# Kernel optimization log

Measured on AMD Instinct MI355X. Metric: run time of the kernel, lower is better.

Reference implementation:

```python
import jax, jax.numpy as jnp
import numpy as np

EPS = 1e-5

def conv1x1(x, W, b):
    # x: [B,C,H,W], W: [O,C], b: [O] -- a 1x1 conv is a per-pixel matmul
    return jnp.einsum('bchw,oc->bohw', x, W) + b[None, :, None, None]

def mean_variance_norm(feat):
    # torch .var(dim=2) is unbiased (ddof=1)
    m = feat.mean(axis=(2, 3), keepdims=True)
    v = feat.var(axis=(2, 3), ddof=1, keepdims=True)
    return (feat - m) / jnp.sqrt(v + EPS)

def setup_inputs() -> dict:
    key = jax.random.key(0)
    ks = jax.random.split(key, 10)
    B, C, H, W = 4, 256, 64, 64
    sc = 1.0 / np.sqrt(C)
    return {
        'content': jax.random.normal(ks[0], (B, C, H, W), jnp.float32),
        'style': jax.random.normal(ks[1], (B, C, H, W), jnp.float32),
        'content_key': jax.random.normal(ks[2], (B, C, H, W), jnp.float32),
        'style_key': jax.random.normal(ks[3], (B, C, H, W), jnp.float32),
        'Wf': jax.random.normal(ks[4], (C, C), jnp.float32) * sc,
        'bf': jnp.zeros((C,), jnp.float32),
        'Wg': jax.random.normal(ks[5], (C, C), jnp.float32) * sc,
        'bg': jnp.zeros((C,), jnp.float32),
        'Wh': jax.random.normal(ks[6], (C, C), jnp.float32) * sc,
        'bh': jnp.zeros((C,), jnp.float32),
    }

def reference(content, style, content_key, style_key, Wf, bf, Wg, bg, Wh, bh):
    Fq = conv1x1(content_key, Wf, bf)   # [B,Ck,H,W]
    G = conv1x1(style_key, Wg, bg)      # [B,Ck,Hs,Ws]
    Hv = conv1x1(style, Wh, bh)         # [B,C,Hs,Ws]
    b, _, h, w = Fq.shape
    _, C, hs, ws = Hv.shape
    N, M = h * w, hs * ws
    q = Fq.reshape(b, -1, N).transpose(0, 2, 1)   # [B,N,Ck]
    k = G.reshape(b, -1, M)                        # [B,Ck,M]
    style_flat = Hv.reshape(b, C, M).transpose(0, 2, 1)  # [B,M,C]
    # masks are all-ones -> attn_mask all zeros -> no masking (faithful to None path)
    S = jax.nn.softmax(jnp.einsum('bnc,bcm->bnm', q, k), axis=-1)  # [B,N,M]
    mean = jnp.einsum('bnm,bmc->bnc', S, style_flat)               # [B,N,C]
    std = jnp.sqrt(jax.nn.relu(
        jnp.einsum('bnm,bmc->bnc', S, style_flat * style_flat) - mean * mean))
    mean = mean.reshape(b, h, w, C).transpose(0, 3, 1, 2)  # [B,C,H,W]
    std = std.reshape(b, h, w, C).transpose(0, 3, 1, 2)
    return std * mean_variance_norm(content) + mean
```

## Files before the change

kernel.cpp:

```cpp
#include <hip/hip_runtime.h>


typedef unsigned int u32;
typedef unsigned short u16;
typedef _Float16 f16x8 __attribute__((ext_vector_type(8)));
typedef float f32x4 __attribute__((ext_vector_type(4)));
typedef float f32x16 __attribute__((ext_vector_type(16)));

#define L2E 1.44269504088896340736f
#define MFMA(a, b, c) __builtin_amdgcn_mfma_f32_16x16x32_f16(a, b, c, 0, 0, 0)
#define MFMA32(a, b, c) __builtin_amdgcn_mfma_f32_32x32x16_f16(a, b, c, 0, 0, 0)
#define EXP2(x) __builtin_amdgcn_exp2f(x)

__device__ __forceinline__ u16 h_bits(_Float16 h) { return __builtin_bit_cast(u16, h); }
__device__ __forceinline__ _Float16 bits_h(u16 x) { return __builtin_bit_cast(_Float16, x); }
__device__ __forceinline__ u16 f2h(float f) { return h_bits((_Float16)f); }

__device__ __forceinline__ f16x8 ldh8(const u16* p) {
    uint4 v = *(const uint4*)p;
    return __builtin_bit_cast(f16x8, v);
}

__global__ void k_stats(const float* __restrict__ content,
                        float* __restrict__ cm, float* __restrict__ cr) {
    int blk = blockIdx.x;
    const float* p = content + (size_t)blk * 4096;
    int t = threadIdx.x;
    float s = 0.f, ss = 0.f;
    for (int i = 0; i < 4; i++) {
        float4 v = *(const float4*)(p + (i * 256 + t) * 4);
        s  += (v.x + v.y) + (v.z + v.w);
        ss += (v.x * v.x + v.y * v.y) + (v.z * v.z + v.w * v.w);
    }
    for (int d = 32; d >= 1; d >>= 1) { s += __shfl_xor(s, d); ss += __shfl_xor(ss, d); }
    __shared__ __align__(16) float as[4], ass[4];
    int w = t >> 6;
    if ((t & 63) == 0) { as[w] = s; ass[w] = ss; }
    __syncthreads();
    if (t == 0) {
        s  = (as[0] + as[1]) + (as[2] + as[3]);
        ss = (ass[0] + ass[1]) + (ass[2] + ass[3]);
        float mean = s * (1.0f / 4096.0f);
        float var = (ss - s * mean) * (1.0f / 4095.0f);
        cm[blk] = mean;
        cr[blk] = rsqrtf(var + 1e-5f);
    }
}

__global__ void k_prep(const float* __restrict__ style, const float* __restrict__ ckey,
                       const float* __restrict__ skey,
                       const float* __restrict__ Wf, const float* __restrict__ Wg,
                       const float* __restrict__ Wh,
                       u16* __restrict__ A, u16* __restrict__ Xq, u16* __restrict__ Cc,
                       u16* __restrict__ Wb) {
    int z = blockIdx.z, t = threadIdx.x;
    if (z >= 12) {
        if (blockIdx.y != 0) return;
        int m = z - 12;
        const float* src = (m == 0) ? Wf : ((m == 1) ? Wg : Wh);
        u16* dst = Wb + m * 65536;
        int i = (blockIdx.x * 256 + t) * 4;
        float4 v = *(const float4*)(src + i);
        ushort4 o;
        o.x = f2h(v.x); o.y = f2h(v.y); o.z = f2h(v.z); o.w = f2h(v.w);
        *(ushort4*)(dst + i) = o;
        return;
    }
    int tensor = z >> 2, b = z & 3;
    const float* src = ((tensor == 0) ? style : ((tensor == 1) ? ckey : skey))
                       + (size_t)b * 256 * 4096;
    u16* dst = ((tensor == 0) ? A : ((tensor == 1) ? Xq : Cc)) + (size_t)b * 4096 * 256;
    int c0 = blockIdx.y * 64, t0 = blockIdx.x * 64;
    __shared__ __align__(16) float ls[64][65];
    int tr = t >> 4, tc = t & 15;
    for (int i = 0; i < 4; i++) {
        int c_off = i * 16 + tr;
        float4 v = *(const float4*)(src + (size_t)(c0 + c_off) * 4096 + t0 + tc * 4);
        ls[tc * 4 + 0][c_off] = v.x;
        ls[tc * 4 + 1][c_off] = v.y;
        ls[tc * 4 + 2][c_off] = v.z;
        ls[tc * 4 + 3][c_off] = v.w;
    }
    __syncthreads();
    for (int i = 0; i < 4; i++) {
        int tokrow = i * 16 + tr;
        ushort4 o;
        o.x = f2h(ls[tokrow][tc * 4 + 0]);
        o.y = f2h(ls[tokrow][tc * 4 + 1]);
        o.z = f2h(ls[tokrow][tc * 4 + 2]);
        o.w = f2h(ls[tokrow][tc * 4 + 3]);
        *(ushort4*)(dst + (size_t)(t0 + tokrow) * 256 + c0 + tc * 4) = o;
    }
}

__launch_bounds__(256, 2)
__global__ void k_gemm_qk(const u16* Xqs, u16* Qd, u16* Xk, const u16* __restrict__ Wb,
                          const float* __restrict__ bfp, const float* __restrict__ bgp) {
    int mode = blockIdx.z, b = blockIdx.y, tok0 = blockIdx.x * 128;
    const u16* X = ((mode == 0) ? Xqs : Xk) + (size_t)b * 4096 * 256;
    u16* O = ((mode == 0) ? Qd : Xk) + (size_t)b * 4096 * 256;
    const u16* W = Wb + mode * 65536;
    const float* bias = (mode == 0) ? bfp : bgp;
    __shared__ __align__(16) u16 wt[256 * 40];
    int t = threadIdx.x, w = t >> 6, lane = t & 63, ln = lane & 15, quad = lane >> 4;

    f32x4 acc[8][4];
    for (int i = 0; i < 8; i++)
        for (int j = 0; j < 4; j++) acc[i][j] = f32x4{0.f, 0.f, 0.f, 0.f};

    for (int ks = 0; ks < 8; ks++) {
        {
            const u16* wr = W + t * 256 + ks * 32;
            uint4 w0 = *(const uint4*)(wr + 0);
            uint4 w1 = *(const uint4*)(wr + 8);
            uint4 w2 = *(const uint4*)(wr + 16);
            uint4 w3 = *(const uint4*)(wr + 24);
            *(uint4*)(wt + t * 40 + 0)  = w0;
            *(uint4*)(wt + t * 40 + 8)  = w1;
            *(uint4*)(wt + t * 40 + 16) = w2;
            *(uint4*)(wt + t * 40 + 24) = w3;
        }
        __syncthreads();
        f16x8 wf[4];
        #pragma unroll
        for (int ct = 0; ct < 4; ct++)
            wf[ct] = ldh8(wt + (w * 64 + ct * 16 + ln) * 40 + quad * 8);
        #pragma unroll
        for (int rt = 0; rt < 8; rt++) {
            f16x8 xf = ldh8(X + (size_t)(tok0 + rt * 16 + ln) * 256 + ks * 32 + quad * 8);
            #pragma unroll
            for (int ct = 0; ct < 4; ct++) acc[rt][ct] = MFMA(xf, wf[ct], acc[rt][ct]);
        }
        __syncthreads();
    }

    float bv[4];
    #pragma unroll
    for (int ct = 0; ct < 4; ct++) bv[ct] = bias[w * 64 + ct * 16 + ln];
    #pragma unroll
    for (int rt = 0; rt < 8; rt++)
        #pragma unroll
        for (int ct = 0; ct < 4; ct++)
            #pragma unroll
            for (int r = 0; r < 4; r++) {
                int tok = tok0 + rt * 16 + quad * 4 + r;
                int o = w * 64 + ct * 16 + ln;
                O[(size_t)tok * 256 + o] = f2h(acc[rt][ct][r] + bv[ct]);
            }
}

__launch_bounds__(256, 2)
__global__ void k_gemm_v(const u16* Xs, const u16* __restrict__ Wh2,
                         const float* __restrict__ bhp, u16* Vt) {
    int b = blockIdx.y, tok0 = blockIdx.x * 128;
    const u16* X = Xs + (size_t)b * 4096 * 256;
    __shared__ __align__(16) u16 wt[256 * 40];
    int t = threadIdx.x, w = t >> 6, lane = t & 63, ln = lane & 15, quad = lane >> 4;

    f32x4 acc[8][4];
    for (int i = 0; i < 8; i++)
        for (int j = 0; j < 4; j++) acc[i][j] = f32x4{0.f, 0.f, 0.f, 0.f};

    for (int ks = 0; ks < 8; ks++) {
        {
            const u16* wr = Wh2 + t * 256 + ks * 32;
            uint4 w0 = *(const uint4*)(wr + 0);
            uint4 w1 = *(const uint4*)(wr + 8);
            uint4 w2 = *(const uint4*)(wr + 16);
            uint4 w3 = *(const uint4*)(wr + 24);
            *(uint4*)(wt + t * 40 + 0)  = w0;
            *(uint4*)(wt + t * 40 + 8)  = w1;
            *(uint4*)(wt + t * 40 + 16) = w2;
            *(uint4*)(wt + t * 40 + 24) = w3;
        }
        __syncthreads();
        f16x8 wf[4];
        #pragma unroll
        for (int ct = 0; ct < 4; ct++)
            wf[ct] = ldh8(wt + (w * 64 + ct * 16 + ln) * 40 + quad * 8);
        #pragma unroll
        for (int rt = 0; rt < 8; rt++) {
            f16x8 xf = ldh8(X + (size_t)(tok0 + rt * 16 + ln) * 256 + ks * 32 + quad * 8);
            #pragma unroll
            for (int ct = 0; ct < 4; ct++) acc[rt][ct] = MFMA(wf[ct], xf, acc[rt][ct]);
        }
        __syncthreads();
    }

    u16* OV = Vt + (size_t)b * 256 * 4096;
    #pragma unroll
    for (int ct = 0; ct < 4; ct++)
        #pragma unroll
        for (int r = 0; r < 4; r++) {
            int o = w * 64 + ct * 16 + quad * 4 + r;
            float bb = bhp[o];
            #pragma unroll
            for (int rt = 0; rt < 8; rt++) {
                int tok = tok0 + rt * 16 + ln;
                OV[(size_t)o * 4096 + tok] = f2h(acc[rt][ct][r] + bb);
            }
        }
}

__launch_bounds__(256, 2)
__global__ void k_flash(const u16* __restrict__ Qt, const u16* __restrict__ Kt,
                        const u16* __restrict__ Vt,
                        const float* __restrict__ content, const float* __restrict__ cm,
                        const float* __restrict__ cr, float* __restrict__ out) {
    __shared__ __align__(16) char smem[79872];
    u16* Ks  = (u16*)smem;
    u16* Vs  = (u16*)(smem + 33792);
    u16* V2h = (u16*)(smem + 43008);
    u16* V2l = (u16*)(smem + 52224);
    int t = threadIdx.x, w = t >> 6, l = t & 63, lq = l & 31, h = l >> 5;
    u16* Psw = (u16*)(smem + 61440) + w * 2304;

    int b = blockIdx.y, q0 = blockIdx.x * 128, coff = blockIdx.z * 64;

    f16x8 qf[16];
    {
        const u16* qp = Qt + ((size_t)b * 4096 + q0 + w * 32 + lq) * 256 + h * 8;
        #pragma unroll
        for (int ks = 0; ks < 16; ks++) qf[ks] = ldh8(qp + ks * 16);
    }

    f32x16 am[2], aq[2];
    #pragma unroll
    for (int i = 0; i < 16; i++) { am[0][i] = 0.f; am[1][i] = 0.f; aq[0][i] = 0.f; aq[1][i] = 0.f; }
    float mrow = -1e30f, lrow = 0.f;

    const u16* Kg = Kt + (size_t)b * 4096 * 256;
    const u16* Vg = Vt + ((size_t)b * 256 + coff) * 4096;

    for (int it = 0; it < 64; it++) {
        int m0 = it * 64;
        #pragma unroll
        for (int i = 0; i < 8; i++) {
            int e = i * 256 + t, row = e >> 5, c16 = e & 31;
            *(uint4*)(Ks + row * 264 + c16 * 8) =
                *(const uint4*)(Kg + (size_t)(m0 + row) * 256 + c16 * 8);
        }
        #pragma unroll
        for (int i = 0; i < 2; i++) {
            int e = i * 256 + t, row = e >> 3, m16 = e & 7;
            uint4 v = *(const uint4*)(Vg + (size_t)row * 4096 + m0 + m16 * 8);
            *(uint4*)(Vs + row * 72 + m16 * 8) = v;
            f16x8 vv = __builtin_bit_cast(f16x8, v);
            f16x8 qh = vv * vv;
            f16x8 ql = __builtin_elementwise_fma(vv, vv, -qh);
            *(uint4*)(V2h + row * 72 + m16 * 8) = __builtin_bit_cast(uint4, qh);
            *(uint4*)(V2l + row * 72 + m16 * 8) = __builtin_bit_cast(uint4, ql);
        }
        __syncthreads();

        f32x16 s0, s1;
        #pragma unroll
        for (int i = 0; i < 16; i++) { s0[i] = 0.f; s1[i] = 0.f; }
        #pragma unroll
        for (int ks = 0; ks < 16; ks++) {
            f16x8 k0 = ldh8(Ks + lq * 264 + ks * 16 + h * 8);
            s0 = MFMA32(k0, qf[ks], s0);
            f16x8 k1 = ldh8(Ks + (32 + lq) * 264 + ks * 16 + h * 8);
            s1 = MFMA32(k1, qf[ks], s1);
        }

        float mt = s0[0];
        #pragma unroll
        for (int r = 1; r < 16; r++) mt = fmaxf(mt, s0[r]);
        #pragma unroll
        for (int r = 0; r < 16; r++) mt = fmaxf(mt, s1[r]);
        mt = fmaxf(mt, __shfl_xor(mt, 32));
        float mn = fmaxf(mrow, mt);
        float al = EXP2((mrow - mn) * L2E);
        mrow = mn;
        float base = mn * L2E;
        float rs = 0.f;
        #pragma unroll
        for (int r = 0; r < 16; r++) {
            float p0 = (float)(_Float16)EXP2(__builtin_fmaf(s0[r], L2E, -base));
            float p1 = (float)(_Float16)EXP2(__builtin_fmaf(s1[r], L2E, -base));
            s0[r] = p0; s1[r] = p1;
            rs += p0 + p1;
        }
        rs += __shfl_xor(rs, 32);
        lrow = lrow * al + rs;

        #pragma unroll
        for (int r = 0; r < 16; r++) {
            float sc = __shfl(al, 8 * (r >> 2) + 4 * h + (r & 3));
            am[0][r] *= sc; am[1][r] *= sc;
            aq[0][r] *= sc; aq[1][r] *= sc;
        }

        #pragma unroll
        for (int mt2 = 0; mt2 < 2; mt2++)
            #pragma unroll
            for (int rq = 0; rq < 4; rq++) {
                float e0 = mt2 ? s1[4 * rq + 0] : s0[4 * rq + 0];
                float e1 = mt2 ? s1[4 * rq + 1] : s0[4 * rq + 1];
                float e2 = mt2 ? s1[4 * rq + 2] : s0[4 * rq + 2];
                float e3 = mt2 ? s1[4 * rq + 3] : s0[4 * rq + 3];
                uint2 pk;
                pk.x = (u32)f2h(e0) | ((u32)f2h(e1) << 16);
                pk.y = (u32)f2h(e2) | ((u32)f2h(e3) << 16);
                *(uint2*)(Psw + lq * 72 + mt2 * 32 + rq * 8 + h * 4) = pk;
            }

        #pragma unroll
        for (int ks = 0; ks < 4; ks++) {
            f16x8 pf = ldh8(Psw + lq * 72 + ks * 16 + h * 8);
            #pragma unroll
            for (int ct = 0; ct < 2; ct++) {
                int vo = (ct * 32 + lq) * 72 + ks * 16 + h * 8;
                am[ct] = MFMA32(pf, ldh8(Vs + vo), am[ct]);
                aq[ct] = MFMA32(pf, ldh8(V2h + vo), aq[ct]);
                aq[ct] = MFMA32(pf, ldh8(V2l + vo), aq[ct]);
            }
        }
        __syncthreads();
    }

    float inv = 1.0f / lrow;
    float iv[16];
    #pragma unroll
    for (int r = 0; r < 16; r++) iv[r] = __shfl(inv, (r & 3) + 8 * (r >> 2) + 4 * h);
    float* Ms = (float*)smem;
    float* Ss = (float*)(smem + 33792);
    #pragma unroll
    for (int ct = 0; ct < 2; ct++)
        #pragma unroll
        for (int rq = 0; rq < 4; rq++) {
            f32x4 mv, sv;
            #pragma unroll
            for (int j = 0; j < 4; j++) {
                int r = 4 * rq + j;
                float mean = am[ct][r] * iv[r];
                float ex2 = aq[ct][r] * iv[r];
                float var = ex2 - mean * mean;
                mv[j] = mean;
                sv[j] = sqrtf(fmaxf(var, 0.f));
            }
            int c = ct * 32 + lq;
            int qloc = w * 32 + 8 * rq + 4 * h;
            *(f32x4*)(Ms + c * 132 + qloc) = mv;
            *(f32x4*)(Ss + c * 132 + qloc) = sv;
        }
    __syncthreads();
    #pragma unroll
    for (int pass = 0; pass < 8; pass++) {
        int c = pass * 8 + (t >> 5);
        int qloc = (t & 31) * 4;
        f32x4 mv = *(const f32x4*)(Ms + c * 132 + qloc);
        f32x4 sv = *(const f32x4*)(Ss + c * 132 + qloc);
        int gc = coff + c;
        size_t basei = ((size_t)b * 256 + gc) * 4096 + q0 + qloc;
        float4 cv = *(const float4*)(content + basei);
        float cmv = cm[b * 256 + gc], crv = cr[b * 256 + gc];
        float4 o;
        o.x = sv[0] * ((cv.x - cmv) * crv) + mv[0];
        o.y = sv[1] * ((cv.y - cmv) * crv) + mv[1];
        o.z = sv[2] * ((cv.z - cmv) * crv) + mv[2];
        o.w = sv[3] * ((cv.w - cmv) * crv) + mv[3];
        *(float4*)(out + basei) = o;
    }
}

extern "C" void kernel_launch(void* const* d_in, const int* in_sizes, int n_in,
                              void* d_out, int out_size, void* d_ws, size_t ws_size,
                              hipStream_t stream) {
    const float* content = (const float*)d_in[0];
    const float* style   = (const float*)d_in[1];
    const float* ckey    = (const float*)d_in[2];
    const float* skey    = (const float*)d_in[3];
    const float* Wf      = (const float*)d_in[4];
    const float* bfp     = (const float*)d_in[5];
    const float* Wg      = (const float*)d_in[6];
    const float* bgp     = (const float*)d_in[7];
    const float* Wh      = (const float*)d_in[8];
    const float* bhp     = (const float*)d_in[9];
    float* out = (float*)d_out;
    char* ws = (char*)d_ws;

    float* cm = (float*)(ws + 0);
    float* cr = (float*)(ws + 4096);
    u16*   Wb = (u16*)(ws + 8192);
    u16*   A  = (u16*)(ws + 1048576);
    u16*   Bv = (u16*)(ws + 9437184);
    u16*   Cc = (u16*)(ws + 17825792);
    u16*   Xq = (u16*)d_out;

    k_stats<<<dim3(1024), 256, 0, stream>>>(content, cm, cr);
    k_prep<<<dim3(64, 4, 15), 256, 0, stream>>>(style, ckey, skey, Wf, Wg, Wh,
                                                A, Xq, Cc, Wb);
    k_gemm_v<<<dim3(32, 4), 256, 0, stream>>>(A, Wb + 2 * 65536, bhp, Bv);
    k_gemm_qk<<<dim3(32, 4, 2), 256, 0, stream>>>(Xq, A, Cc, Wb, bfp, bgp);
    k_flash<<<dim3(32, 4, 4), 256, 0, stream>>>(A, Cc, Bv, content, cm, cr, out);
}
```

Before: 420.9 us.

## Merge projection GEMMs into one launch and compute squared V in-register

The separate V-projection and Q/K-projection GEMM kernels become a single three-mode launch. Staging buffers move into the output area so the V GEMM no longer has to run before the Q GEMM overwrites its input. In the flash kernel, the squared-V high/low split tiles are no longer stored to shared memory each iteration; they are computed from the V fragment right before the MFMAs. This removes one launch and shrinks LDS use, which may allow higher occupancy, at the cost of extra VALU work inside the inner loop.

```diff
diff --git a/kernel.cpp b/kernel.cpp
--- a/kernel.cpp
+++ b/kernel.cpp
@@ -13,7 +13,6 @@
 #define EXP2(x) __builtin_amdgcn_exp2f(x)
 
 __device__ __forceinline__ u16 h_bits(_Float16 h) { return __builtin_bit_cast(u16, h); }
-__device__ __forceinline__ _Float16 bits_h(u16 x) { return __builtin_bit_cast(_Float16, x); }
 __device__ __forceinline__ u16 f2h(float f) { return h_bits((_Float16)f); }
 
 __device__ __forceinline__ f16x8 ldh8(const u16* p) {
@@ -51,7 +50,7 @@
                        const float* __restrict__ skey,
                        const float* __restrict__ Wf, const float* __restrict__ Wg,
                        const float* __restrict__ Wh,
-                       u16* __restrict__ A, u16* __restrict__ Xq, u16* __restrict__ Cc,
+                       u16* __restrict__ X1, u16* __restrict__ X2, u16* __restrict__ Cc,
                        u16* __restrict__ Wb) {
     int z = blockIdx.z, t = threadIdx.x;
     if (z >= 12) {
@@ -69,7 +68,7 @@
     int tensor = z >> 2, b = z & 3;
     const float* src = ((tensor == 0) ? style : ((tensor == 1) ? ckey : skey))
                        + (size_t)b * 256 * 4096;
-    u16* dst = ((tensor == 0) ? A : ((tensor == 1) ? Xq : Cc)) + (size_t)b * 4096 * 256;
+    u16* dst = ((tensor == 0) ? X1 : ((tensor == 1) ? X2 : Cc)) + (size_t)b * 4096 * 256;
     int c0 = blockIdx.y * 64, t0 = blockIdx.x * 64;
     __shared__ __align__(16) float ls[64][65];
     int tr = t >> 4, tc = t & 15;
@@ -94,13 +93,15 @@
 }
 
 __launch_bounds__(256, 2)
-__global__ void k_gemm_qk(const u16* Xqs, u16* Qd, u16* Xk, const u16* __restrict__ Wb,
-                          const float* __restrict__ bfp, const float* __restrict__ bgp) {
+__global__ void k_gemm(const u16* X1, const u16* X2, u16* Cc,
+                       u16* A, u16* Bv, const u16* __restrict__ Wb,
+                       const float* __restrict__ bfp, const float* __restrict__ bgp,
+                       const float* __restrict__ bhp) {
     int mode = blockIdx.z, b = blockIdx.y, tok0 = blockIdx.x * 128;
-    const u16* X = ((mode == 0) ? Xqs : Xk) + (size_t)b * 4096 * 256;
-    u16* O = ((mode == 0) ? Qd : Xk) + (size_t)b * 4096 * 256;
+    const u16* X = ((mode == 0) ? X2 : ((mode == 1) ? (const u16*)Cc : X1))
+                   + (size_t)b * 4096 * 256;
     const u16* W = Wb + mode * 65536;
-    const float* bias = (mode == 0) ? bfp : bgp;
+    const float* bias = (mode == 0) ? bfp : ((mode == 1) ? bgp : bhp);
     __shared__ __align__(16) u16 wt[256 * 40];
     int t = threadIdx.x, w = t >> 6, lane = t & 63, ln = lane & 15, quad = lane >> 4;
 
@@ -128,78 +129,47 @@
         #pragma unroll
         for (int rt = 0; rt < 8; rt++) {
             f16x8 xf = ldh8(X + (size_t)(tok0 + rt * 16 + ln) * 256 + ks * 32 + quad * 8);
-            #pragma unroll
-            for (int ct = 0; ct < 4; ct++) acc[rt][ct] = MFMA(xf, wf[ct], acc[rt][ct]);
+            if (mode < 2) {
+                #pragma unroll
+                for (int ct = 0; ct < 4; ct++) acc[rt][ct] = MFMA(xf, wf[ct], acc[rt][ct]);
+            } else {
+                #pragma unroll
+                for (int ct = 0; ct < 4; ct++) acc[rt][ct] = MFMA(wf[ct], xf, acc[rt][ct]);
+            }
         }
         __syncthreads();
     }
 
-    float bv[4];
-    #pragma unroll
-    for (int ct = 0; ct < 4; ct++) bv[ct] = bias[w * 64 + ct * 16 + ln];
-    #pragma unroll
-    for (int rt = 0; rt < 8; rt++)
+    if (mode < 2) {
+        u16* O = ((mode == 0) ? A : Cc) + (size_t)b * 4096 * 256;
+        float bv[4];
+        #pragma unroll
+        for (int ct = 0; ct < 4; ct++) bv[ct] = bias[w * 64 + ct * 16 + ln];
+        #pragma unroll
+        for (int rt = 0; rt < 8; rt++)
+            #pragma unroll
+            for (int ct = 0; ct < 4; ct++)
+                #pragma unroll
+                for (int r = 0; r < 4; r++) {
+                    int tok = tok0 + rt * 16 + quad * 4 + r;
+                    int o = w * 64 + ct * 16 + ln;
+                    O[(size_t)tok * 256 + o] = f2h(acc[rt][ct][r] + bv[ct]);
+                }
+    } else {
+        u16* OV = Bv + (size_t)b * 256 * 4096;
         #pragma unroll
         for (int ct = 0; ct < 4; ct++)
             #pragma unroll
             for (int r = 0; r < 4; r++) {
-                int tok = tok0 + rt * 16 + quad * 4 + r;
-                int o = w * 64 + ct * 16 + ln;
-                O[(size_t)tok * 256 + o] = f2h(acc[rt][ct][r] + bv[ct]);
-            }
-}
-
-__launch_bounds__(256, 2)
-__global__ void k_gemm_v(const u16* Xs, const u16* __restrict__ Wh2,
-                         const float* __restrict__ bhp, u16* Vt) {
-    int b = blockIdx.y, tok0 = blockIdx.x * 128;
-    const u16* X = Xs + (size_t)b * 4096 * 256;
-    __shared__ __align__(16) u16 wt[256 * 40];
-    int t = threadIdx.x, w = t >> 6, lane = t & 63, ln = lane & 15, quad = lane >> 4;
-
-    f32x4 acc[8][4];
-    for (int i = 0; i < 8; i++)
-        for (int j = 0; j < 4; j++) acc[i][j] = f32x4{0.f, 0.f, 0.f, 0.f};
-
-    for (int ks = 0; ks < 8; ks++) {
-        {
-            const u16* wr = Wh2 + t * 256 + ks * 32;
-            uint4 w0 = *(const uint4*)(wr + 0);
-            uint4 w1 = *(const uint4*)(wr + 8);
-            uint4 w2 = *(const uint4*)(wr + 16);
-            uint4 w3 = *(const uint4*)(wr + 24);
-            *(uint4*)(wt + t * 40 + 0)  = w0;
-            *(uint4*)(wt + t * 40 + 8)  = w1;
-            *(uint4*)(wt + t * 40 + 16) = w2;
-            *(uint4*)(wt + t * 40 + 24) = w3;
-        }
-        __syncthreads();
-        f16x8 wf[4];
-        #pragma unroll
-        for (int ct = 0; ct < 4; ct++)
-            wf[ct] = ldh8(wt + (w * 64 + ct * 16 + ln) * 40 + quad * 8);
-        #pragma unroll
-        for (int rt = 0; rt < 8; rt++) {
-            f16x8 xf = ldh8(X + (size_t)(tok0 + rt * 16 + ln) * 256 + ks * 32 + quad * 8);
-            #pragma unroll
-            for (int ct = 0; ct < 4; ct++) acc[rt][ct] = MFMA(wf[ct], xf, acc[rt][ct]);
-        }
-        __syncthreads();
-    }
-
-    u16* OV = Vt + (size_t)b * 256 * 4096;
-    #pragma unroll
-    for (int ct = 0; ct < 4; ct++)
-        #pragma unroll
-        for (int r = 0; r < 4; r++) {
-            int o = w * 64 + ct * 16 + quad * 4 + r;
-            float bb = bhp[o];
-            #pragma unroll
-            for (int rt = 0; rt < 8; rt++) {
-                int tok = tok0 + rt * 16 + ln;
-                OV[(size_t)o * 4096 + tok] = f2h(acc[rt][ct][r] + bb);
-            }
-        }
+                int o = w * 64 + ct * 16 + quad * 4 + r;
+                float bb = bias[o];
+                #pragma unroll
+                for (int rt = 0; rt < 8; rt++) {
+                    int tok = tok0 + rt * 16 + ln;
+                    OV[(size_t)o * 4096 + tok] = f2h(acc[rt][ct][r] + bb);
+                }
+            }
+    }
 }
 
 __launch_bounds__(256, 2)
@@ -207,13 +177,11 @@
                         const u16* __restrict__ Vt,
                         const float* __restrict__ content, const float* __restrict__ cm,
                         const float* __restrict__ cr, float* __restrict__ out) {
-    __shared__ __align__(16) char smem[79872];
-    u16* Ks  = (u16*)smem;
-    u16* Vs  = (u16*)(smem + 33792);
-    u16* V2h = (u16*)(smem + 43008);
-    u16* V2l = (u16*)(smem + 52224);
+    __shared__ __align__(16) char smem[67584];
+    u16* Ks = (u16*)smem;
+    u16* Vs = (u16*)(smem + 33792);
     int t = threadIdx.x, w = t >> 6, l = t & 63, lq = l & 31, h = l >> 5;
-    u16* Psw = (u16*)(smem + 61440) + w * 2304;
+    u16* Psw = (u16*)(smem + 43008) + w * 2304;
 
     int b = blockIdx.y, q0 = blockIdx.x * 128, coff = blockIdx.z * 64;
 
@@ -243,13 +211,8 @@
         #pragma unroll
         for (int i = 0; i < 2; i++) {
             int e = i * 256 + t, row = e >> 3, m16 = e & 7;
-            uint4 v = *(const uint4*)(Vg + (size_t)row * 4096 + m0 + m16 * 8);
-            *(uint4*)(Vs + row * 72 + m16 * 8) = v;
-            f16x8 vv = __builtin_bit_cast(f16x8, v);
-            f16x8 qh = vv * vv;
-            f16x8 ql = __builtin_elementwise_fma(vv, vv, -qh);
-            *(uint4*)(V2h + row * 72 + m16 * 8) = __builtin_bit_cast(uint4, qh);
-            *(uint4*)(V2l + row * 72 + m16 * 8) = __builtin_bit_cast(uint4, ql);
+            *(uint4*)(Vs + row * 72 + m16 * 8) =
+                *(const uint4*)(Vg + (size_t)row * 4096 + m0 + m16 * 8);
         }
         __syncthreads();
 
@@ -311,10 +274,12 @@
             f16x8 pf = ldh8(Psw + lq * 72 + ks * 16 + h * 8);
             #pragma unroll
             for (int ct = 0; ct < 2; ct++) {
-                int vo = (ct * 32 + lq) * 72 + ks * 16 + h * 8;
-                am[ct] = MFMA32(pf, ldh8(Vs + vo), am[ct]);
-                aq[ct] = MFMA32(pf, ldh8(V2h + vo), aq[ct]);
-                aq[ct] = MFMA32(pf, ldh8(V2l + vo), aq[ct]);
+                f16x8 vf = ldh8(Vs + (ct * 32 + lq) * 72 + ks * 16 + h * 8);
+                am[ct] = MFMA32(pf, vf, am[ct]);
+                f16x8 vh = vf * vf;
+                f16x8 vl = __builtin_elementwise_fma(vf, vf, -vh);
+                aq[ct] = MFMA32(pf, vh, aq[ct]);
+                aq[ct] = MFMA32(pf, vl, aq[ct]);
             }
         }
         __syncthreads();
@@ -387,12 +352,12 @@
     u16*   A  = (u16*)(ws + 1048576);
     u16*   Bv = (u16*)(ws + 9437184);
     u16*   Cc = (u16*)(ws + 17825792);
-    u16*   Xq = (u16*)d_out;
+    u16*   X1 = (u16*)d_out;
+    u16*   X2 = (u16*)d_out + 4194304;
 
     k_stats<<<dim3(1024), 256, 0, stream>>>(content, cm, cr);
     k_prep<<<dim3(64, 4, 15), 256, 0, stream>>>(style, ckey, skey, Wf, Wg, Wh,
-                                                A, Xq, Cc, Wb);
-    k_gemm_v<<<dim3(32, 4), 256, 0, stream>>>(A, Wb + 2 * 65536, bhp, Bv);
-    k_gemm_qk<<<dim3(32, 4, 2), 256, 0, stream>>>(Xq, A, Cc, Wb, bfp, bgp);
+                                                X1, X2, Cc, Wb);
+    k_gemm<<<dim3(32, 4, 3), 256, 0, stream>>>(X1, X2, Cc, A, Bv, Wb, bfp, bgp, bhp);
     k_flash<<<dim3(32, 4, 4), 256, 0, stream>>>(A, Cc, Bv, content, cm, cr, out);
 }
```

Result: no change. 418.0 us (-0.7%).
